# Kernel optimization log

Hardware: AMD Instinct MI355X
Metric: run time of the kernel (lower is better)

The kernel has to match this reference:

```python
import jax, jax.numpy as jnp
import numpy as np

NEG_INF = -1.0e9  # matches the torch code's -1000000000.0 fill


def setup_inputs() -> dict:
    key = jax.random.key(0)
    k1, k2, k3, k4 = jax.random.split(key, 4)
    B, Lq, Lk, D = 8, 2048, 2048, 128
    queries = jax.random.normal(k1, (B, Lq, D), dtype=jnp.float32)
    keys = jax.random.normal(k2, (B, Lk, D), dtype=jnp.float32)
    values = jax.random.normal(k3, (B, Lk, D), dtype=jnp.float32)
    valid_length = jax.random.randint(k4, (B,), 1, Lk + 1, dtype=jnp.int32)
    return {"queries": queries, "keys": keys, "values": values,
            "valid_length": valid_length}


def reference(queries, keys, values, valid_length):
    d = queries.shape[-1]
    # scores: [B, Lq, Lk]
    scores = jnp.einsum("bqd,bkd->bqk", queries, keys) / jnp.sqrt(
        jnp.asarray(d, dtype=queries.dtype))
    # per-batch valid key length broadcast over all queries
    Lk = scores.shape[-1]
    mask = jnp.arange(Lk)[None, None, :] >= valid_length[:, None, None]  # [B,1,Lk]
    scores = jnp.where(mask, NEG_INF, scores)
    attn = jax.nn.softmax(scores, axis=-1)
    # dropout p=0.0 -> identity (eval-equivalent)
    return jnp.einsum("bqk,bkd->bqd", attn, values)
```

## Files before the change

kernel.cpp:

```cpp
#include <hip/hip_runtime.h>


#define NB     8
#define LQ     2048
#define LK     2048
#define DH     128
#define KT     32
#define NSPLIT 4
#define CHUNK  512
#define TPS    16
#define NTILES 64
#define SCL2E  0.12751744f

typedef float f32x4 __attribute__((ext_vector_type(4)));
typedef __bf16 bf16x8 __attribute__((ext_vector_type(8)));
typedef unsigned short u16x4 __attribute__((ext_vector_type(4)));
typedef unsigned short u16x8 __attribute__((ext_vector_type(8)));
typedef unsigned int u32x4 __attribute__((ext_vector_type(4)));

#define KWS_OFF   0ull
#define VWS_OFF   (4ull << 20)
#define OPART_OFF (8ull << 20)
#define ML_OFF    (OPART_OFF + (32ull << 20))
#define WS_NEED   (ML_OFF + 262144ull)

static __device__ __forceinline__ unsigned short f2bf(float f) {
    unsigned int u = __builtin_bit_cast(unsigned int, f);
    u += 0x7FFFu + ((u >> 16) & 1u);
    return (unsigned short)(u >> 16);
}

static __device__ __forceinline__ unsigned int cvtpk(float lo, float hi) {
    unsigned int r;
    asm("v_cvt_pk_bf16_f32 %0, %1, %2" : "=v"(r) : "v"(lo), "v"(hi));
    return r;
}

__global__ __launch_bounds__(256)
void prepass(const float* __restrict__ Kg, const float* __restrict__ Vg,
             const int* __restrict__ VLg,
             unsigned short* __restrict__ Kws, unsigned short* __restrict__ Vws) {
    __shared__ unsigned short Kl[KT][136];
    __shared__ unsigned short Vt[DH][40];
    const int tid = threadIdx.x;
    const int b = blockIdx.x >> 6;
    const int t = blockIdx.x & 63;
    if (t * KT >= VLg[b]) return;
    const size_t gbase = ((size_t)b * LK + (size_t)t * KT) * DH;
    const size_t tbase = (size_t)(b * NTILES + t) * 4096;
    #pragma unroll
    for (int i = 0; i < 4; ++i) {
        int e4 = tid + 256 * i;
        int row = e4 >> 5;
        int c4 = (e4 & 31) * 4;
        float4 kv = *reinterpret_cast<const float4*>(Kg + gbase + (size_t)row * DH + c4);
        u16x4 uk = { f2bf(kv.x), f2bf(kv.y), f2bf(kv.z), f2bf(kv.w) };
        *reinterpret_cast<u16x4*>(&Kl[row][c4]) = uk;
        float4 vv = *reinterpret_cast<const float4*>(Vg + gbase + (size_t)row * DH + c4);
        Vt[c4 + 0][row] = f2bf(vv.x);
        Vt[c4 + 1][row] = f2bf(vv.y);
        Vt[c4 + 2][row] = f2bf(vv.z);
        Vt[c4 + 3][row] = f2bf(vv.w);
    }
    __syncthreads();
    #pragma unroll
    for (int i = 0; i < 2; ++i) {
        int u = tid + 256 * i;
        int sl = u >> 6;
        int l = u & 63;
        int krow = 2 * (l & 15) + (sl & 1);
        int kcol = (sl >> 1) * 32 + (l >> 4) * 8;
        u16x8 kk = *reinterpret_cast<const u16x8*>(&Kl[krow][kcol]);
        *reinterpret_cast<u16x8*>(Kws + tbase + u * 8) = kk;
        int vcol = sl * 16 + (l & 15);
        int k0 = (l >> 4) * 8;
        u16x8 vv8 = *reinterpret_cast<const u16x8*>(&Vt[vcol][k0]);
        *reinterpret_cast<u16x8*>(Vws + tbase + u * 8) = vv8;
    }
}

__global__ __launch_bounds__(64, 2)
void attn_split(const float* __restrict__ Qg, const int* __restrict__ VLg,
                const unsigned short* __restrict__ Kws,
                const unsigned short* __restrict__ Vws,
                float* __restrict__ Opart, float* __restrict__ Ml,
                float* __restrict__ Og) {
    __shared__ unsigned short Plds[2 * 16 * 40];

    const int lane = threadIdx.x;
    const int r    = lane & 15;
    const int grp  = lane >> 4;

    const int bid = blockIdx.x;
    const int b  = bid >> 8;
    const int s  = (bid >> 6) & 3;
    const int qb = bid & 63;

    const int vl = VLg[b];
    if (s * CHUNK >= vl) return;
    int vrem = vl - s * CHUNK;
    if (vrem > CHUNK) vrem = CHUNK;
    const int nt = (vrem + 31) >> 5;
    const bool anymask = (vrem & 31) != 0;
    const int q0 = qb * 32;

    bf16x8 qf0[4], qf1[4];
    #pragma unroll
    for (int rb = 0; rb < 2; ++rb) {
        const float* qrow = Qg + ((size_t)(b * LQ + q0 + rb * 16 + r)) * DH + grp * 8;
        #pragma unroll
        for (int c = 0; c < 4; ++c) {
            float4 f0 = *reinterpret_cast<const float4*>(qrow + c * 32);
            float4 f1 = *reinterpret_cast<const float4*>(qrow + c * 32 + 4);
            u32x4 tw;
            tw[0] = cvtpk(f0.x * SCL2E, f0.y * SCL2E);
            tw[1] = cvtpk(f0.z * SCL2E, f0.w * SCL2E);
            tw[2] = cvtpk(f1.x * SCL2E, f1.y * SCL2E);
            tw[3] = cvtpk(f1.z * SCL2E, f1.w * SCL2E);
            if (rb == 0) qf0[c] = __builtin_bit_cast(bf16x8, tw);
            else         qf1[c] = __builtin_bit_cast(bf16x8, tw);
        }
    }

    const f32x4 zero4 = {0.f, 0.f, 0.f, 0.f};
    f32x4 acc0[8], acc1[8];
    #pragma unroll
    for (int d8 = 0; d8 < 8; ++d8) { acc0[d8] = zero4; acc1[d8] = zero4; }
    float lsum0[4] = {0.f, 0.f, 0.f, 0.f};
    float lsum1[4] = {0.f, 0.f, 0.f, 0.f};

    const unsigned short* kp = Kws + (size_t)(b * NTILES + s * TPS) * 4096 + lane * 8;
    const unsigned short* vp = Vws + (size_t)(b * NTILES + s * TPS) * 4096 + lane * 8;

    bf16x8 kreg[8], vreg[8];
    #pragma unroll
    for (int sl = 0; sl < 8; ++sl) {
        kreg[sl] = *reinterpret_cast<const bf16x8*>(kp + sl * 512);
        vreg[sl] = *reinterpret_cast<const bf16x8*>(vp + sl * 512);
    }

    for (int t = 0; t < nt; ++t) {
        const bool last = (t + 1 == nt);
        f32x4 s00 = zero4, s01 = zero4, s10 = zero4, s11 = zero4;
        #pragma unroll
        for (int c = 0; c < 4; ++c) {
            s00 = __builtin_amdgcn_mfma_f32_16x16x32_bf16(qf0[c], kreg[2 * c],     s00, 0, 0, 0);
            s01 = __builtin_amdgcn_mfma_f32_16x16x32_bf16(qf0[c], kreg[2 * c + 1], s01, 0, 0, 0);
            s10 = __builtin_amdgcn_mfma_f32_16x16x32_bf16(qf1[c], kreg[2 * c],     s10, 0, 0, 0);
            s11 = __builtin_amdgcn_mfma_f32_16x16x32_bf16(qf1[c], kreg[2 * c + 1], s11, 0, 0, 0);
        }
        if (!last) {
            kp += 4096;
            #pragma unroll
            for (int sl = 0; sl < 8; ++sl)
                kreg[sl] = *reinterpret_cast<const bf16x8*>(kp + sl * 512);
        }

        const int kk = s * CHUNK + t * KT + 2 * r;
        const bool mm = last & anymask;
        const bool m0 = mm && (kk >= vl);
        const bool m1 = mm && (kk + 1 >= vl);
        #pragma unroll
        for (int j = 0; j < 4; ++j) {
            float a0 = m0 ? -1e9f : s00[j];
            float a1 = m1 ? -1e9f : s01[j];
            float b0 = m0 ? -1e9f : s10[j];
            float b1 = m1 ? -1e9f : s11[j];
            float p00 = exp2f(a0), p01 = exp2f(a1);
            float p10 = exp2f(b0), p11 = exp2f(b1);
            lsum0[j] += p00 + p01;
            lsum1[j] += p10 + p11;
            *reinterpret_cast<unsigned int*>(&Plds[(grp * 4 + j) * 40 + 2 * r]) =
                cvtpk(p00, p01);
            *reinterpret_cast<unsigned int*>(&Plds[640 + (grp * 4 + j) * 40 + 2 * r]) =
                cvtpk(p10, p11);
        }
        bf16x8 pa0 = *reinterpret_cast<const bf16x8*>(&Plds[r * 40 + grp * 8]);
        bf16x8 pa1 = *reinterpret_cast<const bf16x8*>(&Plds[640 + r * 40 + grp * 8]);

        #pragma unroll
        for (int d8 = 0; d8 < 8; ++d8) {
            acc0[d8] = __builtin_amdgcn_mfma_f32_16x16x32_bf16(pa0, vreg[d8], acc0[d8], 0, 0, 0);
            acc1[d8] = __builtin_amdgcn_mfma_f32_16x16x32_bf16(pa1, vreg[d8], acc1[d8], 0, 0, 0);
        }
        if (!last) {
            vp += 4096;
            #pragma unroll
            for (int sl = 0; sl < 8; ++sl)
                vreg[sl] = *reinterpret_cast<const bf16x8*>(vp + sl * 512);
        }
    }

    #pragma unroll
    for (int j = 0; j < 4; ++j) {
        float v0 = lsum0[j], v1 = lsum1[j];
        #pragma unroll
        for (int d = 1; d < 16; d <<= 1) {
            v0 += __shfl_xor(v0, d);
            v1 += __shfl_xor(v1, d);
        }
        lsum0[j] = v0; lsum1[j] = v1;
    }

    if (vl <= CHUNK) {
        #pragma unroll
        for (int d8 = 0; d8 < 8; ++d8) {
            #pragma unroll
            for (int j = 0; j < 4; ++j) {
                Og[((size_t)(b * LQ + q0 + grp * 4 + j)) * 128 + d8 * 16 + r] =
                    acc0[d8][j] / lsum0[j];
                Og[((size_t)(b * LQ + q0 + 16 + grp * 4 + j)) * 128 + d8 * 16 + r] =
                    acc1[d8][j] / lsum1[j];
            }
        }
    } else {
        const size_t pbase = (size_t)(b * NSPLIT + s) * LQ;
        #pragma unroll
        for (int d8 = 0; d8 < 8; ++d8) {
            #pragma unroll
            for (int j = 0; j < 4; ++j) {
                Opart[(pbase + q0 + grp * 4 + j) * 128 + d8 * 16 + r] = acc0[d8][j];
                Opart[(pbase + q0 + 16 + grp * 4 + j) * 128 + d8 * 16 + r] = acc1[d8][j];
            }
        }
        if (r == 0) {
            #pragma unroll
            for (int j = 0; j < 4; ++j) {
                Ml[pbase + q0 + grp * 4 + j]      = lsum0[j];
                Ml[pbase + q0 + 16 + grp * 4 + j] = lsum1[j];
            }
        }
    }
}

__global__ __launch_bounds__(256)
void reduce_split(const float* __restrict__ Opart, const float* __restrict__ Ml,
                  const int* __restrict__ VLg, float* __restrict__ Og) {
    const int row = blockIdx.x * 8 + (threadIdx.x >> 5);
    const int b = row >> 11;
    const int q = row & 2047;
    const int d4 = (threadIdx.x & 31) * 4;
    const int vl = VLg[b];
    const int ns = min(NSPLIT, (vl + CHUNK - 1) >> 9);
    if (ns <= 1) return;
    float L = 0.f;
    float4 o = {0.f, 0.f, 0.f, 0.f};
    for (int s = 0; s < ns; ++s) {
        size_t i = (size_t)(b * NSPLIT + s) * LQ + q;
        L += Ml[i];
        float4 p = *reinterpret_cast<const float4*>(Opart + i * 128 + d4);
        o.x += p.x; o.y += p.y; o.z += p.z; o.w += p.w;
    }
    float inv = 1.0f / L;
    float4 res = {o.x * inv, o.y * inv, o.z * inv, o.w * inv};
    *reinterpret_cast<float4*>(Og + ((size_t)b * LQ + q) * 128 + d4) = res;
}

#define SCALE 0.08838834764831845f
__global__ __launch_bounds__(256)
void attn_fwd(const float* __restrict__ Qg, const float* __restrict__ Kg,
              const float* __restrict__ Vg, const int* __restrict__ VLg,
              float* __restrict__ Og) {
    __shared__ unsigned short Klds[KT][DH];
    __shared__ unsigned short Vt[DH][KT];
    __shared__ unsigned short Pl[4][16][KT];
    const int tid = threadIdx.x;
    const int lane = tid & 63;
    const int wv = tid >> 6;
    const int r = lane & 15;
    const int grp = lane >> 4;
    const int qblocks = LQ / 64;
    const int b = blockIdx.x / qblocks;
    const int qb = blockIdx.x % qblocks;
    const int q0 = qb * 64 + wv * 16;
    const int vl = VLg[b];
    const int ntiles = (vl + KT - 1) / KT;
    bf16x8 qf[4];
    {
        const float* qrow = Qg + ((size_t)(b * LQ + q0 + r)) * DH + grp * 8;
        #pragma unroll
        for (int c = 0; c < 4; ++c) {
            float4 f0 = *reinterpret_cast<const float4*>(qrow + c * 32);
            float4 f1 = *reinterpret_cast<const float4*>(qrow + c * 32 + 4);
            u16x8 t;
            t[0] = f2bf(f0.x); t[1] = f2bf(f0.y); t[2] = f2bf(f0.z); t[3] = f2bf(f0.w);
            t[4] = f2bf(f1.x); t[5] = f2bf(f1.y); t[6] = f2bf(f1.z); t[7] = f2bf(f1.w);
            qf[c] = __builtin_bit_cast(bf16x8, t);
        }
    }
    const f32x4 zero4 = {0.f, 0.f, 0.f, 0.f};
    f32x4 acc[8];
    #pragma unroll
    for (int d8 = 0; d8 < 8; ++d8) acc[d8] = zero4;
    float mrun[4] = {-1e30f, -1e30f, -1e30f, -1e30f};
    float lsum[4] = {0.f, 0.f, 0.f, 0.f};
    for (int t = 0; t < ntiles; ++t) {
        const int kb = t * KT;
        __syncthreads();
        {
            const size_t kvbase = ((size_t)b * LK + kb) * DH;
            #pragma unroll
            for (int i = 0; i < 4; ++i) {
                int e4 = tid + 256 * i;
                int row = e4 >> 5;
                int c4 = (e4 & 31) * 4;
                float4 kv = *reinterpret_cast<const float4*>(Kg + kvbase + (size_t)row * DH + c4);
                u16x4 uk = { f2bf(kv.x), f2bf(kv.y), f2bf(kv.z), f2bf(kv.w) };
                *reinterpret_cast<u16x4*>(&Klds[row][c4]) = uk;
                float4 vv = *reinterpret_cast<const float4*>(Vg + kvbase + (size_t)row * DH + c4);
                Vt[c4 + 0][row] = f2bf(vv.x);
                Vt[c4 + 1][row] = f2bf(vv.y);
                Vt[c4 + 2][row] = f2bf(vv.z);
                Vt[c4 + 3][row] = f2bf(vv.w);
            }
        }
        __syncthreads();
        f32x4 s0 = zero4, s1 = zero4;
        #pragma unroll
        for (int c = 0; c < 4; ++c) {
            bf16x8 k0 = *reinterpret_cast<const bf16x8*>(&Klds[r][c * 32 + grp * 8]);
            bf16x8 k1 = *reinterpret_cast<const bf16x8*>(&Klds[16 + r][c * 32 + grp * 8]);
            s0 = __builtin_amdgcn_mfma_f32_16x16x32_bf16(qf[c], k0, s0, 0, 0, 0);
            s1 = __builtin_amdgcn_mfma_f32_16x16x32_bf16(qf[c], k1, s1, 0, 0, 0);
        }
        const bool msk0 = (kb + r) >= vl;
        const bool msk1 = (kb + 16 + r) >= vl;
        float alpha[4];
        #pragma unroll
        for (int j = 0; j < 4; ++j) {
            float v0 = msk0 ? -1e9f : s0[j] * SCALE;
            float v1 = msk1 ? -1e9f : s1[j] * SCALE;
            float mx = fmaxf(v0, v1);
            #pragma unroll
            for (int d = 1; d < 16; d <<= 1) mx = fmaxf(mx, __shfl_xor(mx, d));
            float mnew = fmaxf(mrun[j], mx);
            float a = __expf(mrun[j] - mnew);
            float p0 = __expf(v0 - mnew);
            float p1 = __expf(v1 - mnew);
            float rs = p0 + p1;
            #pragma unroll
            for (int d = 1; d < 16; d <<= 1) rs += __shfl_xor(rs, d);
            lsum[j] = lsum[j] * a + rs;
            mrun[j] = mnew;
            alpha[j] = a;
            Pl[wv][grp * 4 + j][r] = f2bf(p0);
            Pl[wv][grp * 4 + j][16 + r] = f2bf(p1);
        }
        #pragma unroll
        for (int d8 = 0; d8 < 8; ++d8) {
            #pragma unroll
            for (int j = 0; j < 4; ++j) acc[d8][j] *= alpha[j];
        }
        bf16x8 pa = *reinterpret_cast<const bf16x8*>(&Pl[wv][r][grp * 8]);
        #pragma unroll
        for (int d8 = 0; d8 < 8; ++d8) {
            bf16x8 vf = *reinterpret_cast<const bf16x8*>(&Vt[d8 * 16 + r][grp * 8]);
            acc[d8] = __builtin_amdgcn_mfma_f32_16x16x32_bf16(pa, vf, acc[d8], 0, 0, 0);
        }
    }
    #pragma unroll
    for (int d8 = 0; d8 < 8; ++d8) {
        #pragma unroll
        for (int j = 0; j < 4; ++j) {
            int qr = q0 + grp * 4 + j;
            Og[((size_t)b * LQ + qr) * DH + d8 * 16 + r] = acc[d8][j] / lsum[j];
        }
    }
}

extern "C" void kernel_launch(void* const* d_in, const int* in_sizes, int n_in,
                              void* d_out, int out_size, void* d_ws, size_t ws_size,
                              hipStream_t stream) {
    const float* Q  = (const float*)d_in[0];
    const float* K  = (const float*)d_in[1];
    const float* V  = (const float*)d_in[2];
    const int*   VL = (const int*)d_in[3];
    float* O = (float*)d_out;

    if (ws_size < WS_NEED) {
        dim3 grid(NB * (LQ / 64));
        attn_fwd<<<grid, 256, 0, stream>>>(Q, K, V, VL, O);
        return;
    }
    unsigned short* Kws = (unsigned short*)((char*)d_ws + KWS_OFF);
    unsigned short* Vws = (unsigned short*)((char*)d_ws + VWS_OFF);
    float* Opart = (float*)((char*)d_ws + OPART_OFF);
    float* Ml    = (float*)((char*)d_ws + ML_OFF);

    prepass<<<dim3(NB * NTILES), 256, 0, stream>>>(K, V, VL, Kws, Vws);
    attn_split<<<dim3(NB * NSPLIT * 64), 64, 0, stream>>>(
        Q, VL, Kws, Vws, Opart, Ml, O);
    reduce_split<<<dim3(NB * LQ / 8), 256, 0, stream>>>(Opart, Ml, VL, O);
}
```

Baseline: 43.18 us.

## Process 64 query rows per wave with Q staged in swizzled LDS

Each single-wave block now handles 64 query rows instead of 32, halving the grid so every K/V tile loaded into registers is reused across four 16-row MFMA blocks. Q fragments are converted to bf16 once and kept in a rotated-column LDS buffer rather than in registers, and P is staged two row-blocks at a time. This halves K/V global traffic per query, at the cost of 16 KB of extra LDS per block, 128 accumulator registers per lane and fewer blocks to spread across the CUs.

```diff
diff --git a/kernel.cpp b/kernel.cpp
--- a/kernel.cpp
+++ b/kernel.cpp
@@ -85,6 +85,7 @@
                 const unsigned short* __restrict__ Vws,
                 float* __restrict__ Opart, float* __restrict__ Ml,
                 float* __restrict__ Og) {
+    __shared__ unsigned short Qlds[64 * 128];
     __shared__ unsigned short Plds[2 * 16 * 40];
 
     const int lane = threadIdx.x;
@@ -92,9 +93,9 @@
     const int grp  = lane >> 4;
 
     const int bid = blockIdx.x;
-    const int b  = bid >> 8;
-    const int s  = (bid >> 6) & 3;
-    const int qb = bid & 63;
+    const int b  = bid >> 7;
+    const int s  = (bid >> 5) & 3;
+    const int qb = bid & 31;
 
     const int vl = VLg[b];
     if (s * CHUNK >= vl) return;
@@ -102,32 +103,35 @@
     if (vrem > CHUNK) vrem = CHUNK;
     const int nt = (vrem + 31) >> 5;
     const bool anymask = (vrem & 31) != 0;
-    const int q0 = qb * 32;
-
-    bf16x8 qf0[4], qf1[4];
-    #pragma unroll
-    for (int rb = 0; rb < 2; ++rb) {
-        const float* qrow = Qg + ((size_t)(b * LQ + q0 + rb * 16 + r)) * DH + grp * 8;
-        #pragma unroll
-        for (int c = 0; c < 4; ++c) {
-            float4 f0 = *reinterpret_cast<const float4*>(qrow + c * 32);
-            float4 f1 = *reinterpret_cast<const float4*>(qrow + c * 32 + 4);
+    const int q0 = qb * 64;
+
+    {
+        const float* qrow = Qg + ((size_t)(b * LQ + q0 + lane)) * DH;
+        #pragma unroll
+        for (int sl = 0; sl < 16; ++sl) {
+            float4 f0 = *reinterpret_cast<const float4*>(qrow + sl * 8);
+            float4 f1 = *reinterpret_cast<const float4*>(qrow + sl * 8 + 4);
             u32x4 tw;
             tw[0] = cvtpk(f0.x * SCL2E, f0.y * SCL2E);
             tw[1] = cvtpk(f0.z * SCL2E, f0.w * SCL2E);
             tw[2] = cvtpk(f1.x * SCL2E, f1.y * SCL2E);
             tw[3] = cvtpk(f1.z * SCL2E, f1.w * SCL2E);
-            if (rb == 0) qf0[c] = __builtin_bit_cast(bf16x8, tw);
-            else         qf1[c] = __builtin_bit_cast(bf16x8, tw);
+            int ps = (sl + lane) & 15;
+            *reinterpret_cast<u32x4*>(&Qlds[lane * 128 + ps * 8]) = tw;
         }
     }
 
     const f32x4 zero4 = {0.f, 0.f, 0.f, 0.f};
-    f32x4 acc0[8], acc1[8];
-    #pragma unroll
-    for (int d8 = 0; d8 < 8; ++d8) { acc0[d8] = zero4; acc1[d8] = zero4; }
-    float lsum0[4] = {0.f, 0.f, 0.f, 0.f};
-    float lsum1[4] = {0.f, 0.f, 0.f, 0.f};
+    f32x4 acc[4][8];
+    #pragma unroll
+    for (int rb = 0; rb < 4; ++rb)
+        #pragma unroll
+        for (int d8 = 0; d8 < 8; ++d8) acc[rb][d8] = zero4;
+    float lsum[4][4];
+    #pragma unroll
+    for (int rb = 0; rb < 4; ++rb)
+        #pragma unroll
+        for (int j = 0; j < 4; ++j) lsum[rb][j] = 0.f;
 
     const unsigned short* kp = Kws + (size_t)(b * NTILES + s * TPS) * 4096 + lane * 8;
     const unsigned short* vp = Vws + (size_t)(b * NTILES + s * TPS) * 4096 + lane * 8;
@@ -141,13 +145,20 @@
 
     for (int t = 0; t < nt; ++t) {
         const bool last = (t + 1 == nt);
-        f32x4 s00 = zero4, s01 = zero4, s10 = zero4, s11 = zero4;
+
+        f32x4 st[4][2];
+        #pragma unroll
+        for (int rb = 0; rb < 4; ++rb) { st[rb][0] = zero4; st[rb][1] = zero4; }
         #pragma unroll
         for (int c = 0; c < 4; ++c) {
-            s00 = __builtin_amdgcn_mfma_f32_16x16x32_bf16(qf0[c], kreg[2 * c],     s00, 0, 0, 0);
-            s01 = __builtin_amdgcn_mfma_f32_16x16x32_bf16(qf0[c], kreg[2 * c + 1], s01, 0, 0, 0);
-            s10 = __builtin_amdgcn_mfma_f32_16x16x32_bf16(qf1[c], kreg[2 * c],     s10, 0, 0, 0);
-            s11 = __builtin_amdgcn_mfma_f32_16x16x32_bf16(qf1[c], kreg[2 * c + 1], s11, 0, 0, 0);
+            #pragma unroll
+            for (int rb = 0; rb < 4; ++rb) {
+                int row = rb * 16 + r;
+                bf16x8 q = *reinterpret_cast<const bf16x8*>(
+                    &Qlds[row * 128 + ((c * 4 + grp + row) & 15) * 8]);
+                st[rb][0] = __builtin_amdgcn_mfma_f32_16x16x32_bf16(q, kreg[2 * c],     st[rb][0], 0, 0, 0);
+                st[rb][1] = __builtin_amdgcn_mfma_f32_16x16x32_bf16(q, kreg[2 * c + 1], st[rb][1], 0, 0, 0);
+            }
         }
         if (!last) {
             kp += 4096;
@@ -161,27 +172,27 @@
         const bool m0 = mm && (kk >= vl);
         const bool m1 = mm && (kk + 1 >= vl);
         #pragma unroll
-        for (int j = 0; j < 4; ++j) {
-            float a0 = m0 ? -1e9f : s00[j];
-            float a1 = m1 ? -1e9f : s01[j];
-            float b0 = m0 ? -1e9f : s10[j];
-            float b1 = m1 ? -1e9f : s11[j];
-            float p00 = exp2f(a0), p01 = exp2f(a1);
-            float p10 = exp2f(b0), p11 = exp2f(b1);
-            lsum0[j] += p00 + p01;
-            lsum1[j] += p10 + p11;
-            *reinterpret_cast<unsigned int*>(&Plds[(grp * 4 + j) * 40 + 2 * r]) =
-                cvtpk(p00, p01);
-            *reinterpret_cast<unsigned int*>(&Plds[640 + (grp * 4 + j) * 40 + 2 * r]) =
-                cvtpk(p10, p11);
-        }
-        bf16x8 pa0 = *reinterpret_cast<const bf16x8*>(&Plds[r * 40 + grp * 8]);
-        bf16x8 pa1 = *reinterpret_cast<const bf16x8*>(&Plds[640 + r * 40 + grp * 8]);
-
-        #pragma unroll
-        for (int d8 = 0; d8 < 8; ++d8) {
-            acc0[d8] = __builtin_amdgcn_mfma_f32_16x16x32_bf16(pa0, vreg[d8], acc0[d8], 0, 0, 0);
-            acc1[d8] = __builtin_amdgcn_mfma_f32_16x16x32_bf16(pa1, vreg[d8], acc1[d8], 0, 0, 0);
+        for (int h = 0; h < 2; ++h) {
+            #pragma unroll
+            for (int rbh = 0; rbh < 2; ++rbh) {
+                const int rb = h * 2 + rbh;
+                #pragma unroll
+                for (int j = 0; j < 4; ++j) {
+                    float a0 = m0 ? -1e9f : st[rb][0][j];
+                    float a1 = m1 ? -1e9f : st[rb][1][j];
+                    float p0 = exp2f(a0), p1 = exp2f(a1);
+                    lsum[rb][j] += p0 + p1;
+                    *reinterpret_cast<unsigned int*>(
+                        &Plds[rbh * 640 + (grp * 4 + j) * 40 + 2 * r]) = cvtpk(p0, p1);
+                }
+            }
+            bf16x8 paA = *reinterpret_cast<const bf16x8*>(&Plds[r * 40 + grp * 8]);
+            bf16x8 paB = *reinterpret_cast<const bf16x8*>(&Plds[640 + r * 40 + grp * 8]);
+            #pragma unroll
+            for (int d8 = 0; d8 < 8; ++d8) {
+                acc[h * 2][d8]     = __builtin_amdgcn_mfma_f32_16x16x32_bf16(paA, vreg[d8], acc[h * 2][d8], 0, 0, 0);
+                acc[h * 2 + 1][d8] = __builtin_amdgcn_mfma_f32_16x16x32_bf16(paB, vreg[d8], acc[h * 2 + 1][d8], 0, 0, 0);
+            }
         }
         if (!last) {
             vp += 4096;
@@ -192,43 +203,47 @@
     }
 
     #pragma unroll
-    for (int j = 0; j < 4; ++j) {
-        float v0 = lsum0[j], v1 = lsum1[j];
-        #pragma unroll
-        for (int d = 1; d < 16; d <<= 1) {
-            v0 += __shfl_xor(v0, d);
-            v1 += __shfl_xor(v1, d);
-        }
-        lsum0[j] = v0; lsum1[j] = v1;
+    for (int rb = 0; rb < 4; ++rb) {
+        #pragma unroll
+        for (int j = 0; j < 4; ++j) {
+            float v = lsum[rb][j];
+            #pragma unroll
+            for (int d = 1; d < 16; d <<= 1) v += __shfl_xor(v, d);
+            lsum[rb][j] = v;
+        }
     }
 
     if (vl <= CHUNK) {
         #pragma unroll
-        for (int d8 = 0; d8 < 8; ++d8) {
-            #pragma unroll
-            for (int j = 0; j < 4; ++j) {
-                Og[((size_t)(b * LQ + q0 + grp * 4 + j)) * 128 + d8 * 16 + r] =
-                    acc0[d8][j] / lsum0[j];
-                Og[((size_t)(b * LQ + q0 + 16 + grp * 4 + j)) * 128 + d8 * 16 + r] =
-                    acc1[d8][j] / lsum1[j];
+        for (int rb = 0; rb < 4; ++rb) {
+            #pragma unroll
+            for (int d8 = 0; d8 < 8; ++d8) {
+                #pragma unroll
+                for (int j = 0; j < 4; ++j) {
+                    Og[((size_t)(b * LQ + q0 + rb * 16 + grp * 4 + j)) * 128 + d8 * 16 + r] =
+                        acc[rb][d8][j] / lsum[rb][j];
+                }
             }
         }
     } else {
         const size_t pbase = (size_t)(b * NSPLIT + s) * LQ;
         #pragma unroll
-        for (int d8 = 0; d8 < 8; ++d8) {
-            #pragma unroll
-            for (int j = 0; j < 4; ++j) {
-                Opart[(pbase + q0 + grp * 4 + j) * 128 + d8 * 16 + r] = acc0[d8][j];
-                Opart[(pbase + q0 + 16 + grp * 4 + j) * 128 + d8 * 16 + r] = acc1[d8][j];
+        for (int rb = 0; rb < 4; ++rb) {
+            #pragma unroll
+            for (int d8 = 0; d8 < 8; ++d8) {
+                #pragma unroll
+                for (int j = 0; j < 4; ++j) {
+                    Opart[(pbase + q0 + rb * 16 + grp * 4 + j) * 128 + d8 * 16 + r] =
+                        acc[rb][d8][j];
+                }
             }
         }
         if (r == 0) {
             #pragma unroll
-            for (int j = 0; j < 4; ++j) {
-                Ml[pbase + q0 + grp * 4 + j]      = lsum0[j];
-                Ml[pbase + q0 + 16 + grp * 4 + j] = lsum1[j];
-            }
+            for (int rb = 0; rb < 4; ++rb)
+                #pragma unroll
+                for (int j = 0; j < 4; ++j)
+                    Ml[pbase + q0 + rb * 16 + grp * 4 + j] = lsum[rb][j];
         }
     }
 }
@@ -388,7 +403,7 @@
     float* Ml    = (float*)((char*)d_ws + ML_OFF);
 
     prepass<<<dim3(NB * NTILES), 256, 0, stream>>>(K, V, VL, Kws, Vws);
-    attn_split<<<dim3(NB * NSPLIT * 64), 64, 0, stream>>>(
+    attn_split<<<dim3(NB * NSPLIT * 32), 64, 0, stream>>>(
         Q, VL, Kws, Vws, Opart, Ml, O);
     reduce_split<<<dim3(NB * LQ / 8), 256, 0, stream>>>(Opart, Ml, VL, O);
 }
```

Result: slower. 114.3 us (+164.8%).

## Split key tiles across two waves per block and combine partials in LDS

Applied to the files above, without the earlier changes.

Each attention block now runs two wavefronts, and they process alternating 32-key tiles of the chunk. At the end, wave 1 writes its accumulators and row sums to shared memory, and wave 0 adds them and writes the output. This halves the serial tile loop per wave and puts more waves in flight to hide load and MFMA latency. In exchange it adds a shared-memory combine, two block barriers and a larger LDS footprint. Because no running max is kept and the query is pre-scaled, the two partial results can be added directly.

```diff
diff --git a/kernel.cpp b/kernel.cpp
--- a/kernel.cpp
+++ b/kernel.cpp
@@ -79,17 +79,21 @@
     }
 }
 
-__global__ __launch_bounds__(64, 2)
+__global__ __launch_bounds__(128, 2)
 void attn_split(const float* __restrict__ Qg, const int* __restrict__ VLg,
                 const unsigned short* __restrict__ Kws,
                 const unsigned short* __restrict__ Vws,
                 float* __restrict__ Opart, float* __restrict__ Ml,
                 float* __restrict__ Og) {
-    __shared__ unsigned short Plds[2 * 16 * 40];
-
-    const int lane = threadIdx.x;
+    __shared__ __align__(16) char shbuf[16640];
+
+    const int tid  = threadIdx.x;
+    const int lane = tid & 63;
+    const int wv   = tid >> 6;
     const int r    = lane & 15;
     const int grp  = lane >> 4;
+
+    unsigned short* Plds = reinterpret_cast<unsigned short*>(shbuf) + wv * 1280;
 
     const int bid = blockIdx.x;
     const int b  = bid >> 8;
@@ -123,14 +127,17 @@
     }
 
     const f32x4 zero4 = {0.f, 0.f, 0.f, 0.f};
-    f32x4 acc0[8], acc1[8];
-    #pragma unroll
-    for (int d8 = 0; d8 < 8; ++d8) { acc0[d8] = zero4; acc1[d8] = zero4; }
-    float lsum0[4] = {0.f, 0.f, 0.f, 0.f};
-    float lsum1[4] = {0.f, 0.f, 0.f, 0.f};
-
-    const unsigned short* kp = Kws + (size_t)(b * NTILES + s * TPS) * 4096 + lane * 8;
-    const unsigned short* vp = Vws + (size_t)(b * NTILES + s * TPS) * 4096 + lane * 8;
+    f32x4 acc[2][8];
+    #pragma unroll
+    for (int rb = 0; rb < 2; ++rb)
+        #pragma unroll
+        for (int d8 = 0; d8 < 8; ++d8) acc[rb][d8] = zero4;
+    float lsum[2][4] = {{0.f, 0.f, 0.f, 0.f}, {0.f, 0.f, 0.f, 0.f}};
+
+    const unsigned short* kp =
+        Kws + (size_t)(b * NTILES + s * TPS + wv) * 4096 + lane * 8;
+    const unsigned short* vp =
+        Vws + (size_t)(b * NTILES + s * TPS + wv) * 4096 + lane * 8;
 
     bf16x8 kreg[8], vreg[8];
     #pragma unroll
@@ -139,8 +146,8 @@
         vreg[sl] = *reinterpret_cast<const bf16x8*>(vp + sl * 512);
     }
 
-    for (int t = 0; t < nt; ++t) {
-        const bool last = (t + 1 == nt);
+    for (int t = wv; t < nt; t += 2) {
+        const bool lastt = (t == nt - 1);
         f32x4 s00 = zero4, s01 = zero4, s10 = zero4, s11 = zero4;
         #pragma unroll
         for (int c = 0; c < 4; ++c) {
@@ -149,15 +156,15 @@
             s10 = __builtin_amdgcn_mfma_f32_16x16x32_bf16(qf1[c], kreg[2 * c],     s10, 0, 0, 0);
             s11 = __builtin_amdgcn_mfma_f32_16x16x32_bf16(qf1[c], kreg[2 * c + 1], s11, 0, 0, 0);
         }
-        if (!last) {
-            kp += 4096;
+        if (t + 2 < nt) {
+            kp += 2 * 4096;
             #pragma unroll
             for (int sl = 0; sl < 8; ++sl)
                 kreg[sl] = *reinterpret_cast<const bf16x8*>(kp + sl * 512);
         }
 
         const int kk = s * CHUNK + t * KT + 2 * r;
-        const bool mm = last & anymask;
+        const bool mm = lastt & anymask;
         const bool m0 = mm && (kk >= vl);
         const bool m1 = mm && (kk + 1 >= vl);
         #pragma unroll
@@ -168,8 +175,8 @@
             float b1 = m1 ? -1e9f : s11[j];
             float p00 = exp2f(a0), p01 = exp2f(a1);
             float p10 = exp2f(b0), p11 = exp2f(b1);
-            lsum0[j] += p00 + p01;
-            lsum1[j] += p10 + p11;
+            lsum[0][j] += p00 + p01;
+            lsum[1][j] += p10 + p11;
             *reinterpret_cast<unsigned int*>(&Plds[(grp * 4 + j) * 40 + 2 * r]) =
                 cvtpk(p00, p01);
             *reinterpret_cast<unsigned int*>(&Plds[640 + (grp * 4 + j) * 40 + 2 * r]) =
@@ -180,11 +187,11 @@
 
         #pragma unroll
         for (int d8 = 0; d8 < 8; ++d8) {
-            acc0[d8] = __builtin_amdgcn_mfma_f32_16x16x32_bf16(pa0, vreg[d8], acc0[d8], 0, 0, 0);
-            acc1[d8] = __builtin_amdgcn_mfma_f32_16x16x32_bf16(pa1, vreg[d8], acc1[d8], 0, 0, 0);
-        }
-        if (!last) {
-            vp += 4096;
+            acc[0][d8] = __builtin_amdgcn_mfma_f32_16x16x32_bf16(pa0, vreg[d8], acc[0][d8], 0, 0, 0);
+            acc[1][d8] = __builtin_amdgcn_mfma_f32_16x16x32_bf16(pa1, vreg[d8], acc[1][d8], 0, 0, 0);
+        }
+        if (t + 2 < nt) {
+            vp += 2 * 4096;
             #pragma unroll
             for (int sl = 0; sl < 8; ++sl)
                 vreg[sl] = *reinterpret_cast<const bf16x8*>(vp + sl * 512);
@@ -192,43 +199,76 @@
     }
 
     #pragma unroll
-    for (int j = 0; j < 4; ++j) {
-        float v0 = lsum0[j], v1 = lsum1[j];
-        #pragma unroll
-        for (int d = 1; d < 16; d <<= 1) {
-            v0 += __shfl_xor(v0, d);
-            v1 += __shfl_xor(v1, d);
-        }
-        lsum0[j] = v0; lsum1[j] = v1;
+    for (int rb = 0; rb < 2; ++rb) {
+        #pragma unroll
+        for (int j = 0; j < 4; ++j) {
+            float v = lsum[rb][j];
+            #pragma unroll
+            for (int d = 1; d < 16; d <<= 1) v += __shfl_xor(v, d);
+            lsum[rb][j] = v;
+        }
+    }
+
+    __syncthreads();
+    float* Cmb = reinterpret_cast<float*>(shbuf);
+    float* Ls  = reinterpret_cast<float*>(shbuf + 16384);
+    if (wv == 1) {
+        #pragma unroll
+        for (int rb = 0; rb < 2; ++rb) {
+            #pragma unroll
+            for (int d8 = 0; d8 < 8; ++d8) {
+                int ps = ((rb * 8 + d8) + lane) & 15;
+                *reinterpret_cast<f32x4*>(&Cmb[lane * 64 + ps * 4]) = acc[rb][d8];
+            }
+        }
+        if (r == 0) {
+            #pragma unroll
+            for (int rb = 0; rb < 2; ++rb)
+                #pragma unroll
+                for (int j = 0; j < 4; ++j)
+                    Ls[rb * 16 + grp * 4 + j] = lsum[rb][j];
+        }
+    }
+    __syncthreads();
+    if (wv != 0) return;
+
+    #pragma unroll
+    for (int rb = 0; rb < 2; ++rb) {
+        #pragma unroll
+        for (int d8 = 0; d8 < 8; ++d8) {
+            int ps = ((rb * 8 + d8) + lane) & 15;
+            f32x4 o = *reinterpret_cast<const f32x4*>(&Cmb[lane * 64 + ps * 4]);
+            acc[rb][d8] += o;
+        }
+        #pragma unroll
+        for (int j = 0; j < 4; ++j) lsum[rb][j] += Ls[rb * 16 + grp * 4 + j];
     }
 
     if (vl <= CHUNK) {
         #pragma unroll
-        for (int d8 = 0; d8 < 8; ++d8) {
-            #pragma unroll
-            for (int j = 0; j < 4; ++j) {
-                Og[((size_t)(b * LQ + q0 + grp * 4 + j)) * 128 + d8 * 16 + r] =
-                    acc0[d8][j] / lsum0[j];
-                Og[((size_t)(b * LQ + q0 + 16 + grp * 4 + j)) * 128 + d8 * 16 + r] =
-                    acc1[d8][j] / lsum1[j];
-            }
-        }
+        for (int rb = 0; rb < 2; ++rb)
+            #pragma unroll
+            for (int d8 = 0; d8 < 8; ++d8)
+                #pragma unroll
+                for (int j = 0; j < 4; ++j)
+                    Og[((size_t)(b * LQ + q0 + rb * 16 + grp * 4 + j)) * 128 + d8 * 16 + r] =
+                        acc[rb][d8][j] / lsum[rb][j];
     } else {
         const size_t pbase = (size_t)(b * NSPLIT + s) * LQ;
         #pragma unroll
-        for (int d8 = 0; d8 < 8; ++d8) {
-            #pragma unroll
-            for (int j = 0; j < 4; ++j) {
-                Opart[(pbase + q0 + grp * 4 + j) * 128 + d8 * 16 + r] = acc0[d8][j];
-                Opart[(pbase + q0 + 16 + grp * 4 + j) * 128 + d8 * 16 + r] = acc1[d8][j];
-            }
-        }
+        for (int rb = 0; rb < 2; ++rb)
+            #pragma unroll
+            for (int d8 = 0; d8 < 8; ++d8)
+                #pragma unroll
+                for (int j = 0; j < 4; ++j)
+                    Opart[(pbase + q0 + rb * 16 + grp * 4 + j) * 128 + d8 * 16 + r] =
+                        acc[rb][d8][j];
         if (r == 0) {
             #pragma unroll
-            for (int j = 0; j < 4; ++j) {
-                Ml[pbase + q0 + grp * 4 + j]      = lsum0[j];
-                Ml[pbase + q0 + 16 + grp * 4 + j] = lsum1[j];
-            }
+            for (int rb = 0; rb < 2; ++rb)
+                #pragma unroll
+                for (int j = 0; j < 4; ++j)
+                    Ml[pbase + q0 + rb * 16 + grp * 4 + j] = lsum[rb][j];
         }
     }
 }
@@ -388,7 +428,7 @@
     float* Ml    = (float*)((char*)d_ws + ML_OFF);
 
     prepass<<<dim3(NB * NTILES), 256, 0, stream>>>(K, V, VL, Kws, Vws);
-    attn_split<<<dim3(NB * NSPLIT * 64), 64, 0, stream>>>(
+    attn_split<<<dim3(NB * NSPLIT * 64), 128, 0, stream>>>(
         Q, VL, Kws, Vws, Opart, Ml, O);
     reduce_split<<<dim3(NB * LQ / 8), 256, 0, stream>>>(Opart, Ml, VL, O);
 }
```

New measurement: 43.05 us. About the same (-0.3%).
